# Performance work log

Hardware: AMD Instinct MI355X
Metric: run time of the kernel (lower is better)

## Reference

```python
import jax, jax.numpy as jnp
import numpy as np

N_LAYERS = 8
DILATIONS = [1, 2, 1, 2, 1, 2, 1, 2]
K_HOPS = 3
BN = 13248   # batch(64) * n_nodes(207), merged as in the torch module
L = 13       # 12 history steps + 1; shrinks by sum(dilations)=12 across layers
E = 211968   # BN * avg_degree(16)


def _conv1d(x, w, b, dil):
    # x: (BN, Cin, L), w: (Cout, Cin, 2) kernel-2 dilated conv, VALID (causal shrink)
    y = jax.lax.conv_general_dilated(x, w, (1,), 'VALID', rhs_dilation=(dil,),
                                     dimension_numbers=('NCH', 'OIH', 'NCH'))
    return y + b[None, :, None]


def setup_inputs() -> dict:
    key = jax.random.key(0)
    ks = jax.random.split(key, 20)
    s = 0.1  # keep activations in a sane range
    return {
        'x': jax.random.normal(ks[0], (BN, L, 2), jnp.float32),
        'edge_src': jax.random.randint(ks[1], (E,), 0, BN),
        'edge_dst': jax.random.randint(ks[2], (E,), 0, BN),
        'edge_w': jax.random.uniform(ks[3], (E,), jnp.float32),
        'init_w': s * jax.random.normal(ks[4], (2, 32), jnp.float32),
        'init_b': s * jax.random.normal(ks[5], (32,), jnp.float32),
        'filt_w': s * jax.random.normal(ks[6], (8, 32, 32, 2), jnp.float32),
        'filt_b': s * jax.random.normal(ks[7], (8, 32), jnp.float32),
        'gate_w': s * jax.random.normal(ks[8], (8, 32, 32, 2), jnp.float32),
        'gate_b': s * jax.random.normal(ks[9], (8, 32), jnp.float32),
        'gcn_w': s * jax.random.normal(ks[10], (8, 6, 32, 32), jnp.float32),
        'gcn_b': s * jax.random.normal(ks[11], (8, 32), jnp.float32),
        'skip_w': s * jax.random.normal(ks[12], (8, 256, 32), jnp.float32),
        'skip_b': s * jax.random.normal(ks[13], (8, 256), jnp.float32),
        'out0_w': s * jax.random.normal(ks[14], (256, 512), jnp.float32),
        'out0_b': s * jax.random.normal(ks[15], (512,), jnp.float32),
        'out1_w': s * jax.random.normal(ks[16], (512, 12), jnp.float32),
        'out1_b': s * jax.random.normal(ks[17], (12,), jnp.float32),
    }


def reference(x, edge_src, edge_dst, edge_w, init_w, init_b,
              filt_w, filt_b, gate_w, gate_b, gcn_w, gcn_b,
              skip_w, skip_b, out0_w, out0_b, out1_w, out1_b):
    # init linear: (BN, L, 2) -> (BN, L, 32) -> (BN, 32, L)
    h = (x @ init_w + init_b).transpose(0, 2, 1)
    # per-hop edge weights: elementwise powers of the transition weights
    # (faithful to repo's dense_to_sparse(transition ** k)); bck = transposed edges
    adjs = [(edge_src, edge_dst, edge_w ** k) for k in range(1, K_HOPS + 1)] + \
           [(edge_dst, edge_src, edge_w ** k) for k in range(1, K_HOPS + 1)]
    skip = None
    for l in range(N_LAYERS):
        d = DILATIONS[l]
        res = h
        # Gated TCN: tanh(filter) * sigmoid(gate), seq shrinks by d
        t = jnp.tanh(_conv1d(h, filt_w[l], filt_b[l], d)) * \
            jax.nn.sigmoid(_conv1d(h, gate_w[l], gate_b[l], d))
        # Diffusion conv: sum over 6 adjacency types of A_w (x W_a)
        xt = t.transpose(0, 2, 1)  # (BN, L', 32)
        g = jnp.zeros_like(xt)
        for a, (src, dst, w) in enumerate(adjs):
            msg = (xt @ gcn_w[l, a])[src] * w[:, None, None]  # (E, L', 32)
            g = g + jax.ops.segment_sum(msg, dst, num_segments=BN)
        h = g.transpose(0, 2, 1) + gcn_b[l][None, :, None]  # (BN, 32, L')
        # residual connection (align shrunk sequence)
        h = h + res[:, :, -h.shape[-1]:]
        # skip conv (1x1) on last timestep, accumulated
        sc = h[:, :, -1] @ skip_w[l].T + skip_b[l]  # (BN, 256)
        skip = sc if skip is None else skip + sc
    out = jax.nn.relu(skip)
    out = jax.nn.relu(out @ out0_w + out0_b)
    return out @ out1_w + out1_b  # (BN, 12)
```

## Files before the change

kernel.cpp:

```cpp
#include <hip/hip_runtime.h>
#include <hip/hip_fp16.h>

#define BN 13248
#define NE 211968
#define ZSTRIDE 200
#define HSTRIDE 40
#define HNODE 480

typedef __attribute__((ext_vector_type(8))) short bf16x8;
typedef __attribute__((ext_vector_type(8))) _Float16 f16x8;
typedef __attribute__((ext_vector_type(4))) float f32x4;

__device__ __forceinline__ f32x4 mfma16b(bf16x8 a, bf16x8 b, f32x4 c) {
  return __builtin_amdgcn_mfma_f32_16x16x32_bf16(a, b, c, 0, 0, 0);
}
__device__ __forceinline__ f32x4 mfma16h(f16x8 a, f16x8 b, f32x4 c) {
  return __builtin_amdgcn_mfma_f32_16x16x32_f16(a, b, c, 0, 0, 0);
}

__device__ __forceinline__ unsigned short to_bf16(float v) {
  unsigned bits = __float_as_uint(v);
  return (unsigned short)((bits + 0x7FFFu + ((bits >> 16) & 1u)) >> 16);
}
__device__ __forceinline__ unsigned short to_f16(float v) {
  union { __half h; unsigned short s; } u; u.h = __float2half(v); return u.s;
}
__device__ __forceinline__ unsigned h2u(__half2 h) {
  union { __half2 h; unsigned u; } v; v.h = h; return v.u;
}
__device__ __forceinline__ __half2 u2h(unsigned u) {
  union { unsigned u; __half2 h; } v; v.u = u; return v.h;
}

__device__ __forceinline__ float fast_tanh(float x) {
  float e2 = __expf(2.f * x);
  return 1.f - 2.f / (e2 + 1.f);
}
__device__ __forceinline__ float fast_sig(float x) {
  return 1.f / (1.f + __expf(-x));
}

__global__ void k_count(const int* __restrict__ src, const int* __restrict__ dst,
                        int* __restrict__ cur_f, int* __restrict__ cur_b) {
  int e = blockIdx.x * 256 + threadIdx.x;
  if (e < NE) {
    atomicAdd(&cur_f[dst[e]], 1);
    atomicAdd(&cur_b[src[e]], 1);
  }
}

__global__ void k_scan(int* __restrict__ cur_f, int* __restrict__ row_f,
                       int* __restrict__ cur_b, int* __restrict__ row_b) {
  __shared__ int sdata[1024];
  int tid = threadIdx.x;
  for (int which = 0; which < 2; ++which) {
    int* cnt = which ? cur_b : cur_f;
    int* row = which ? row_b : row_f;
    int base = tid * 13;
    int vals[13];
    int tot = 0;
    for (int k = 0; k < 13; ++k) {
      int idx = base + k;
      int v = (idx < BN) ? cnt[idx] : 0;
      vals[k] = v; tot += v;
    }
    sdata[tid] = tot;
    __syncthreads();
    for (int off = 1; off < 1024; off <<= 1) {
      int add = (tid >= off) ? sdata[tid - off] : 0;
      __syncthreads();
      sdata[tid] += add;
      __syncthreads();
    }
    int running = sdata[tid] - tot;
    for (int k = 0; k < 13; ++k) {
      int idx = base + k;
      if (idx < BN) { row[idx] = running; cnt[idx] = running; running += vals[k]; }
    }
    if (tid == 1023) row[BN] = sdata[1023];
    __syncthreads();
  }
}

__global__ void k_fill(const int* __restrict__ src, const int* __restrict__ dst,
                       const float* __restrict__ w,
                       int* __restrict__ cur_f, int4* __restrict__ ce_f,
                       int* __restrict__ cur_b, int4* __restrict__ ce_b) {
  int e = blockIdx.x * 256 + threadIdx.x;
  if (e < NE) {
    int s = src[e], t = dst[e];
    float wv = w[e];
    float w2 = wv * wv, w3 = w2 * wv;
    int u1 = (int)h2u(__float2half2_rn(wv));
    int u2 = (int)h2u(__float2half2_rn(w2));
    int u3 = (int)h2u(__float2half2_rn(w3));
    int p = atomicAdd(&cur_f[t], 1); ce_f[p] = make_int4(s, u1, u2, u3);
    int q = atomicAdd(&cur_b[s], 1); ce_b[q] = make_int4(t, u1, u2, u3);
  }
}

__global__ void k_init(const float* __restrict__ x, const float* __restrict__ iw,
                       const float* __restrict__ ib, float* __restrict__ h) {
  int idx = blockIdx.x * 256 + threadIdx.x;
  if (idx >= BN * 13 * 32) return;
  int c = idx & 31;
  int r = idx >> 5;
  int n = r % BN;
  int tau = r / BN;
  float x0 = x[(n * 13 + tau) * 2 + 0];
  float x1 = x[(n * 13 + tau) * 2 + 1];
  h[idx] = fmaf(x0, iw[c], fmaf(x1, iw[32 + c], ib[c]));
}

__global__ void k_pack(const float* __restrict__ skip_w, const float* __restrict__ skip_b,
                       const float* __restrict__ w0, const float* __restrict__ w1,
                       const float* __restrict__ gcn_w,
                       const float* __restrict__ filt_w, const float* __restrict__ gate_w,
                       unsigned short* __restrict__ SWb, unsigned short* __restrict__ W0T,
                       unsigned short* __restrict__ W1T, float* __restrict__ bsum,
                       unsigned short* __restrict__ Gg16, unsigned short* __restrict__ WTC) {
  int id = blockIdx.x * 256 + threadIdx.x;
  if (id < 65536) {
    int j = id >> 8, k = id & 255;
    SWb[id] = to_bf16(skip_w[((k >> 5) * 256 + j) * 32 + (k & 31)]);
  }
  if (id < 131072) {
    int jo = id >> 8, k = id & 255;
    W0T[id] = to_bf16(w0[k * 512 + jo]);
  }
  if (id < 8192) {
    int n = id >> 9, k = id & 511;
    W1T[id] = (n < 12) ? to_bf16(w1[k * 12 + n]) : (unsigned short)0;
  }
  if (id < 256) {
    float s = 0.f;
    for (int l = 0; l < 8; ++l) s += skip_b[l * 256 + id];
    bsum[id] = s;
  }
  if (id < 49152) {
    int l = id / 6144, rem = id % 6144;
    int co = rem / 192, k = rem % 192;
    int a = k >> 5, ci = k & 31;
    Gg16[id] = to_f16(gcn_w[((l * 6 + a) * 32 + ci) * 32 + co]);
  }
  if (id < 32768) {
    int l = id >> 12, rem = id & 4095;
    int g = rem >> 11, co = (rem >> 6) & 31, k = rem & 63;
    const float* srcw = (g ? gate_w : filt_w) + l * 2048;
    float v = (k < 32) ? srcw[(co * 32 + k) * 2 + 0] : srcw[(co * 32 + (k - 32)) * 2 + 1];
    WTC[id] = to_f16(v);
  }
}

template<int LIN, int D, int TPAD>
__global__ __launch_bounds__(256) void k_tcn(const float* __restrict__ h_in, unsigned short* __restrict__ t_out,
    const float* __restrict__ fw, const float* __restrict__ fb,
    const float* __restrict__ gw, const float* __restrict__ gb) {
  constexpr int LOUT = LIN - D;
  __shared__ __align__(16) float wq[32 * 32 * 4];
  __shared__ float hl[8][LIN * 32];
  int tid = threadIdx.x;
  for (int f = tid; f < 4096; f += 256) {
    int e = f & 3, co = (f >> 2) & 31, ci = f >> 7;
    const float* srcw = (e < 2) ? fw : gw;
    wq[f] = srcw[(co * 32 + ci) * 2 + (e & 1)];
  }
  int n0 = blockIdx.x * 8;
  for (int i = tid; i < 8 * LIN * 32; i += 256) {
    int c = i & 31, r = i >> 5;
    int nl = r / LIN, tau = r % LIN;
    hl[nl][tau * 32 + c] = h_in[(tau * BN + n0 + nl) * 32 + c];
  }
  __syncthreads();
  int nl = tid >> 5, co = tid & 31;
  int n = n0 + nl;
  float accf[LOUT], accg[LOUT];
  float fbv = fb[co], gbv = gb[co];
#pragma unroll
  for (int j = 0; j < LOUT; ++j) { accf[j] = fbv; accg[j] = gbv; }
#pragma unroll
  for (int ci = 0; ci < 32; ++ci) {
    float4 wv = *(const float4*)&wq[(ci * 32 + co) * 4];
    float xr[LIN];
#pragma unroll
    for (int t = 0; t < LIN; ++t) xr[t] = hl[nl][t * 32 + ci];
#pragma unroll
    for (int j = 0; j < LOUT; ++j) {
      accf[j] = fmaf(xr[j], wv.x, accf[j]);
      accf[j] = fmaf(xr[j + D], wv.y, accf[j]);
      accg[j] = fmaf(xr[j], wv.z, accg[j]);
      accg[j] = fmaf(xr[j + D], wv.w, accg[j]);
    }
  }
#pragma unroll
  for (int j = 0; j < TPAD; ++j) {
    unsigned short v = 0;
    if (j < LOUT) v = to_f16(fast_tanh(accf[j < LOUT ? j : 0]) * fast_sig(accg[j < LOUT ? j : 0]));
    t_out[(n * TPAD + j) * 32 + co] = v;
  }
}

template<int TPAD, int NT>
__device__ __forceinline__ void edge_fma(const int4& c, const uint2 (&u)[NT], __half2* A) {
  __half2 wh0 = u2h((unsigned)c.y), wh1 = u2h((unsigned)c.z), wh2 = u2h((unsigned)c.w);
#pragma unroll
  for (int j = 0; j < NT; ++j) {
    __half2 v0 = u2h(u[j].x), v1 = u2h(u[j].y);
    A[(0 * NT + j) * 2 + 0] = __hfma2(wh0, v0, A[(0 * NT + j) * 2 + 0]);
    A[(0 * NT + j) * 2 + 1] = __hfma2(wh0, v1, A[(0 * NT + j) * 2 + 1]);
    A[(1 * NT + j) * 2 + 0] = __hfma2(wh1, v0, A[(1 * NT + j) * 2 + 0]);
    A[(1 * NT + j) * 2 + 1] = __hfma2(wh1, v1, A[(1 * NT + j) * 2 + 1]);
    A[(2 * NT + j) * 2 + 0] = __hfma2(wh2, v0, A[(2 * NT + j) * 2 + 0]);
    A[(2 * NT + j) * 2 + 1] = __hfma2(wh2, v1, A[(2 * NT + j) * 2 + 1]);
  }
}

template<int TPAD, int NT>
__device__ __forceinline__ void gather_dir(const unsigned short* __restrict__ t_in,
    int e0, int e1, const int4* __restrict__ ce, int rowoff0, __half2* A) {
  constexpr int EB = 4;
  int e = e0;
  for (; e + EB <= e1; e += EB) {
    int4 c[EB];
    uint2 u[EB][NT];
#pragma unroll
    for (int k = 0; k < EB; ++k) c[k] = ce[e + k];
#pragma unroll
    for (int k = 0; k < EB; ++k) {
      const unsigned short* p = t_in + c[k].x * (TPAD * 32) + rowoff0;
#pragma unroll
      for (int j = 0; j < NT; ++j) u[k][j] = *(const uint2*)(p + j * 32);
    }
#pragma unroll
    for (int k = 0; k < EB; ++k) edge_fma<TPAD, NT>(c[k], u[k], A);
  }
  for (; e < e1; ++e) {
    int4 c = ce[e];
    uint2 u[NT];
    const unsigned short* p = t_in + c.x * (TPAD * 32) + rowoff0;
#pragma unroll
    for (int j = 0; j < NT; ++j) u[j] = *(const uint2*)(p + j * 32);
    edge_fma<TPAD, NT>(c, u, A);
  }
}

template<int LOUT, int D, int TPAD, int D2, int TPAD2, bool LAST>
__global__ __launch_bounds__(128, 4) void k_fused(
    const unsigned short* __restrict__ t_in,
    const float* __restrict__ h_in, float* __restrict__ h_out,
    float* __restrict__ lastcol, unsigned short* __restrict__ t_next,
    const int* __restrict__ row_f, const int4* __restrict__ ce_f,
    const int* __restrict__ row_b, const int4* __restrict__ ce_b,
    const unsigned short* __restrict__ Wg,
    const float* __restrict__ bias,
    const unsigned short* __restrict__ Wtc,
    const float* __restrict__ fbn, const float* __restrict__ gbn) {
  constexpr int NT = TPAD / 4;
  constexpr int LOUT2 = LAST ? 1 : (LOUT - D2);
  constexpr int SBYTES = 4 * TPAD * ZSTRIDE * 2;
  __shared__ __align__(16) char smem[SBYTES];
  unsigned short* Zl = (unsigned short*)smem;
  unsigned short* hb16 = (unsigned short*)smem;
  int tid = threadIdx.x;
  int nl = tid >> 5, lane32 = tid & 31;
  int tl = lane32 >> 3;
  int c4 = (lane32 & 7) << 2;
  int n0 = blockIdx.x * 4;
  int n = n0 + nl;
  int rowoff0 = (tl * NT) * 32 + c4;
  int ef0 = row_f[n], ef1 = row_f[n + 1];
  int eb0 = row_b[n], eb1 = row_b[n + 1];
  __half2 acc[6 * NT * 2];
  __half2 zero = __float2half2_rn(0.f);
#pragma unroll
  for (int i = 0; i < 6 * NT * 2; ++i) acc[i] = zero;
  gather_dir<TPAD, NT>(t_in, ef0, ef1, ce_f, rowoff0, acc);
  gather_dir<TPAD, NT>(t_in, eb0, eb1, ce_b, rowoff0, acc + 3 * NT * 2);
#pragma unroll
  for (int j = 0; j < NT; ++j) {
    int m = nl * TPAD + tl * NT + j;
#pragma unroll
    for (int a = 0; a < 6; ++a) {
      uint2 v = make_uint2(h2u(acc[(a * NT + j) * 2 + 0]), h2u(acc[(a * NT + j) * 2 + 1]));
      *(uint2*)(&Zl[m * ZSTRIDE + a * 32 + c4]) = v;
    }
  }
  __syncthreads();
  int wave = tid >> 6, lane = tid & 63;
  int m16 = lane & 15, q = lane >> 4;
  f32x4 dacc[NT];
#pragma unroll
  for (int i = 0; i < NT; ++i) {
    int u = wave * NT + i;
    int mt = u >> 1, nt = u & 1;
    dacc[i] = (f32x4){0.f, 0.f, 0.f, 0.f};
#pragma unroll
    for (int ks = 0; ks < 6; ++ks) {
      f16x8 av = *(const f16x8*)(&Zl[(mt * 16 + m16) * ZSTRIDE + ks * 32 + q * 8]);
      f16x8 bv = *(const f16x8*)((const _Float16*)Wg + (nt * 16 + m16) * 192 + ks * 32 + q * 8);
      dacc[i] = mfma16h(av, bv, dacc[i]);
    }
  }
  __syncthreads();
#pragma unroll
  for (int i = 0; i < NT; ++i) {
    int u = wave * NT + i;
    int mt = u >> 1, nt = u & 1;
    int co = nt * 16 + m16;
    float bco = bias[co];
#pragma unroll
    for (int r = 0; r < 4; ++r) {
      int mm = mt * 16 + q * 4 + r;
      int node = mm / TPAD;
      int tau = mm % TPAD;
      if (tau < LOUT) {
        float rres = h_in[((tau + D) * BN + n0 + node) * 32 + co];
        float o = dacc[i][r] + bco + rres;
        h_out[(tau * BN + n0 + node) * 32 + co] = o;
        if (!LAST) hb16[node * HNODE + tau * HSTRIDE + co] = to_f16(o);
        if (tau == LOUT - 1) lastcol[(n0 + node) * 32 + co] = o;
      }
    }
  }
  if (!LAST) {
    __syncthreads();
#pragma unroll
    for (int i = 0; i < 4; ++i) {
      int u = wave * 4 + i;
      int node = u >> 1, ntc = u & 1;
      int co = ntc * 16 + m16;
      f32x4 df = (f32x4){0.f, 0.f, 0.f, 0.f};
      f32x4 dg = (f32x4){0.f, 0.f, 0.f, 0.f};
#pragma unroll
      for (int s = 0; s < 2; ++s) {
        f16x8 av = *(const f16x8*)(&hb16[node * HNODE + (m16 + s * D2) * HSTRIDE + q * 8]);
        f16x8 bvf = *(const f16x8*)((const _Float16*)Wtc + (0 * 32 + co) * 64 + s * 32 + q * 8);
        f16x8 bvg = *(const f16x8*)((const _Float16*)Wtc + (1 * 32 + co) * 64 + s * 32 + q * 8);
        df = mfma16h(av, bvf, df);
        dg = mfma16h(av, bvg, dg);
      }
      float fbv = fbn[co], gbv = gbn[co];
#pragma unroll
      for (int r = 0; r < 4; ++r) {
        int j = q * 4 + r;
        if (j < TPAD2) {
          unsigned short v = 0;
          if (j < LOUT2)
            v = to_f16(fast_tanh(df[r] + fbv) * fast_sig(dg[r] + gbv));
          t_next[((n0 + node) * TPAD2 + j) * 32 + co] = v;
        }
      }
    }
  }
}

__device__ __forceinline__ bf16x8 ldsA(const unsigned short* buf, int stride, int row, int ks, int q) {
  int unit = ks * 4 + q;
  int addr = row * stride + ((unit ^ (row & 7)) << 3);
  return *(const bf16x8*)(buf + addr);
}

__global__ __launch_bounds__(256) void k_final(const float* __restrict__ lastcol,
    const unsigned short* __restrict__ SWb, const unsigned short* __restrict__ W0T,
    const unsigned short* __restrict__ W1T, const float* __restrict__ bsum,
    const float* __restrict__ b0, const float* __restrict__ b1,
    float* __restrict__ out) {
  __shared__ __align__(16) unsigned short Z[32 * 256];
  __shared__ __align__(16) unsigned short H[32 * 512];
  int tid = threadIdx.x;
  int wave = tid >> 6, lane = tid & 63;
  int m16 = lane & 15, q = lane >> 4;
  int n0 = blockIdx.x * 32;
#pragma unroll
  for (int it = 0; it < 32; ++it) {
    int id = it * 256 + tid;
    int m = id >> 8, k = id & 255;
    float v = lastcol[((k >> 5) * BN + n0 + m) * 32 + (k & 31)];
    Z[m * 256 + (((k >> 3) ^ (m & 7)) << 3) + (k & 7)] = to_bf16(v);
  }
  __syncthreads();
  f32x4 acc1[2][4];
#pragma unroll
  for (int mt = 0; mt < 2; ++mt)
#pragma unroll
    for (int i = 0; i < 4; ++i) acc1[mt][i] = (f32x4){0.f, 0.f, 0.f, 0.f};
#pragma unroll
  for (int ks = 0; ks < 8; ++ks) {
    bf16x8 a0 = ldsA(Z, 256, m16, ks, q);
    bf16x8 a1 = ldsA(Z, 256, 16 + m16, ks, q);
#pragma unroll
    for (int i = 0; i < 4; ++i) {
      int j = (wave * 4 + i) * 16 + m16;
      bf16x8 b = *(const bf16x8*)(SWb + j * 256 + ks * 32 + q * 8);
      acc1[0][i] = mfma16b(a0, b, acc1[0][i]);
      acc1[1][i] = mfma16b(a1, b, acc1[1][i]);
    }
  }
  __syncthreads();
#pragma unroll
  for (int i = 0; i < 4; ++i) {
    int j = (wave * 4 + i) * 16 + m16;
    float bs = bsum[j];
#pragma unroll
    for (int mt = 0; mt < 2; ++mt)
#pragma unroll
      for (int r = 0; r < 4; ++r) {
        int row = mt * 16 + q * 4 + r;
        float v = fmaxf(acc1[mt][i][r] + bs, 0.f);
        Z[row * 256 + (((j >> 3) ^ (row & 7)) << 3) + (j & 7)] = to_bf16(v);
      }
  }
  __syncthreads();
  f32x4 acc2[2][8];
#pragma unroll
  for (int mt = 0; mt < 2; ++mt)
#pragma unroll
    for (int i = 0; i < 8; ++i) acc2[mt][i] = (f32x4){0.f, 0.f, 0.f, 0.f};
#pragma unroll
  for (int ks = 0; ks < 8; ++ks) {
    bf16x8 a0 = ldsA(Z, 256, m16, ks, q);
    bf16x8 a1 = ldsA(Z, 256, 16 + m16, ks, q);
#pragma unroll
    for (int i = 0; i < 8; ++i) {
      int jo = (wave * 8 + i) * 16 + m16;
      bf16x8 b = *(const bf16x8*)(W0T + jo * 256 + ks * 32 + q * 8);
      acc2[0][i] = mfma16b(a0, b, acc2[0][i]);
      acc2[1][i] = mfma16b(a1, b, acc2[1][i]);
    }
  }
#pragma unroll
  for (int i = 0; i < 8; ++i) {
    int jo = (wave * 8 + i) * 16 + m16;
    float b0v = b0[jo];
#pragma unroll
    for (int mt = 0; mt < 2; ++mt)
#pragma unroll
      for (int r = 0; r < 4; ++r) {
        int row = mt * 16 + q * 4 + r;
        float v = fmaxf(acc2[mt][i][r] + b0v, 0.f);
        H[row * 512 + (((jo >> 3) ^ (row & 7)) << 3) + (jo & 7)] = to_bf16(v);
      }
  }
  __syncthreads();
  if (wave < 2) {
    f32x4 acc3 = (f32x4){0.f, 0.f, 0.f, 0.f};
#pragma unroll
    for (int ks = 0; ks < 16; ++ks) {
      bf16x8 a = ldsA(H, 512, wave * 16 + m16, ks, q);
      bf16x8 b = *(const bf16x8*)(W1T + m16 * 512 + ks * 32 + q * 8);
      acc3 = mfma16b(a, b, acc3);
    }
    if (m16 < 12) {
      float bv = b1[m16];
#pragma unroll
      for (int r = 0; r < 4; ++r)
        out[(n0 + wave * 16 + q * 4 + r) * 12 + m16] = acc3[r] + bv;
    }
  }
}

extern "C" void kernel_launch(void* const* d_in, const int* in_sizes, int n_in,
                              void* d_out, int out_size, void* d_ws, size_t ws_size,
                              hipStream_t stream) {
  const float* x      = (const float*)d_in[0];
  const int*   esrc   = (const int*)d_in[1];
  const int*   edst   = (const int*)d_in[2];
  const float* ew     = (const float*)d_in[3];
  const float* init_w = (const float*)d_in[4];
  const float* init_b = (const float*)d_in[5];
  const float* filt_w = (const float*)d_in[6];
  const float* filt_b = (const float*)d_in[7];
  const float* gate_w = (const float*)d_in[8];
  const float* gate_b = (const float*)d_in[9];
  const float* gcn_w  = (const float*)d_in[10];
  const float* gcn_b  = (const float*)d_in[11];
  const float* skip_w = (const float*)d_in[12];
  const float* skip_b = (const float*)d_in[13];
  const float* w0     = (const float*)d_in[14];
  const float* b0     = (const float*)d_in[15];
  const float* w1     = (const float*)d_in[16];
  const float* b1     = (const float*)d_in[17];
  float* out = (float*)d_out;

  float* base = (float*)d_ws;
  float* hA      = base;
  float* hB      = hA + 13 * BN * 32;
  unsigned short* tA = (unsigned short*)(hB + 13 * BN * 32);
  unsigned short* tB = tA + 12 * BN * 32;
  float* lastcol = (float*)(tB + 12 * BN * 32);
  int* row_f = (int*)(lastcol + 8 * BN * 32);
  int* row_b = row_f + (BN + 2);
  int* cur_f = row_b + (BN + 2);
  int* cur_b = cur_f + BN;
  int4* ce_f = (int4*)(cur_b + BN + 2);
  int4* ce_b = ce_f + NE;
  unsigned short* SWb  = (unsigned short*)(ce_b + NE);
  unsigned short* W0T  = SWb + 65536;
  unsigned short* W1T  = W0T + 131072;
  unsigned short* Gg16 = W1T + 8192;
  unsigned short* WTC  = Gg16 + 49152;
  float* bsumv = (float*)(WTC + 32768);

  hipMemsetAsync(cur_f, 0, 2 * BN * sizeof(int), stream);
  const int egrid = (NE + 255) / 256;
  k_count<<<egrid, 256, 0, stream>>>(esrc, edst, cur_f, cur_b);
  k_scan<<<1, 1024, 0, stream>>>(cur_f, row_f, cur_b, row_b);
  k_fill<<<egrid, 256, 0, stream>>>(esrc, edst, ew, cur_f, ce_f, cur_b, ce_b);
  k_init<<<(BN * 13 * 32 + 255) / 256, 256, 0, stream>>>(x, init_w, init_b, hA);
  k_pack<<<512, 256, 0, stream>>>(skip_w, skip_b, w0, w1, gcn_w, filt_w, gate_w,
                                  SWb, W0T, W1T, bsumv, Gg16, WTC);

  k_tcn<13, 1, 12><<<BN / 8, 256, 0, stream>>>(hA, tA, filt_w, filt_b, gate_w, gate_b);

#define FUSED(l, LOUTv, Dv, TPv, D2v, TP2v, LASTv, tin, tout, hin, hout) \
  k_fused<LOUTv, Dv, TPv, D2v, TP2v, LASTv><<<BN / 4, 128, 0, stream>>>( \
      tin, hin, hout, lastcol + l * BN * 32, tout, row_f, ce_f, row_b, ce_b, \
      Gg16 + l * 6144, gcn_b + l * 32, WTC + (l + 1) * 4096, \
      filt_b + (l + 1) * 32, gate_b + (l + 1) * 32);

  FUSED(0, 12, 1, 12, 2, 12, false, tA, tB, hA, hB)
  FUSED(1, 10, 2, 12, 1, 12, false, tB, tA, hB, hA)
  FUSED(2,  9, 1, 12, 2,  8, false, tA, tB, hA, hB)
  FUSED(3,  7, 2,  8, 1,  8, false, tB, tA, hB, hA)
  FUSED(4,  6, 1,  8, 2,  4, false, tA, tB, hA, hB)
  FUSED(5,  4, 2,  4, 1,  4, false, tB, tA, hB, hA)
  FUSED(6,  3, 1,  4, 2,  4, false, tA, tB, hA, hB)
#undef FUSED
  k_fused<1, 2, 4, 2, 4, true><<<BN / 4, 128, 0, stream>>>(
      tB, hB, hA, lastcol + 7 * BN * 32, tA, row_f, ce_f, row_b, ce_b,
      Gg16 + 7 * 6144, gcn_b + 7 * 32, WTC, filt_b, gate_b);

  k_final<<<BN / 32, 256, 0, stream>>>(lastcol, SWb, W0T, W1T, bsumv, b0, b1, out);
}
```

Baseline: 684.3 us.

## Bucket CSR edges by neighbor index range and skip padded row loads

Edge counting, scan and fill now use 8 sub-buckets per node keyed by the high bits of the neighbor index, so each node's edge list is roughly sorted by source node. This should make the gathers in the fused layer kernels touch memory with better locality and L2 reuse. The gather also skips loading padded time rows beyond the valid output length when the padded size exceeds it. In exchange the scan runs over 8x more counters in a single block, and the count and fill atomics are spread over a larger array.

```diff
diff --git a/kernel.cpp b/kernel.cpp
--- a/kernel.cpp
+++ b/kernel.cpp
@@ -3,6 +3,7 @@
 
 #define BN 13248
 #define NE 211968
+#define NBKT 8
 #define ZSTRIDE 200
 #define HSTRIDE 40
 #define HNODE 480
@@ -44,25 +45,26 @@
                         int* __restrict__ cur_f, int* __restrict__ cur_b) {
   int e = blockIdx.x * 256 + threadIdx.x;
   if (e < NE) {
-    atomicAdd(&cur_f[dst[e]], 1);
-    atomicAdd(&cur_b[src[e]], 1);
-  }
-}
-
-__global__ void k_scan(int* __restrict__ cur_f, int* __restrict__ row_f,
-                       int* __restrict__ cur_b, int* __restrict__ row_b) {
+    int s = src[e], t = dst[e];
+    atomicAdd(&cur_f[t * NBKT + (s >> 11)], 1);
+    atomicAdd(&cur_b[s * NBKT + (t >> 11)], 1);
+  }
+}
+
+__global__ void k_scan(int* __restrict__ cnt_f, int* __restrict__ row_f,
+                       int* __restrict__ cnt_b, int* __restrict__ row_b) {
   __shared__ int sdata[1024];
+  const int TOT = BN * NBKT;
+  const int PER = (TOT + 1023) / 1024;
   int tid = threadIdx.x;
   for (int which = 0; which < 2; ++which) {
-    int* cnt = which ? cur_b : cur_f;
+    int* cnt = which ? cnt_b : cnt_f;
     int* row = which ? row_b : row_f;
-    int base = tid * 13;
-    int vals[13];
+    int base = tid * PER;
     int tot = 0;
-    for (int k = 0; k < 13; ++k) {
+    for (int k = 0; k < PER; ++k) {
       int idx = base + k;
-      int v = (idx < BN) ? cnt[idx] : 0;
-      vals[k] = v; tot += v;
+      if (idx < TOT) tot += cnt[idx];
     }
     sdata[tid] = tot;
     __syncthreads();
@@ -73,11 +75,16 @@
       __syncthreads();
     }
     int running = sdata[tid] - tot;
-    for (int k = 0; k < 13; ++k) {
+    for (int k = 0; k < PER; ++k) {
       int idx = base + k;
-      if (idx < BN) { row[idx] = running; cnt[idx] = running; running += vals[k]; }
-    }
-    if (tid == 1023) row[BN] = sdata[1023];
+      if (idx < TOT) {
+        int v = cnt[idx];
+        if ((idx & (NBKT - 1)) == 0) row[idx / NBKT] = running;
+        cnt[idx] = running;
+        running += v;
+      }
+    }
+    if (tid == 1023) row[BN] = NE;
     __syncthreads();
   }
 }
@@ -94,8 +101,8 @@
     int u1 = (int)h2u(__float2half2_rn(wv));
     int u2 = (int)h2u(__float2half2_rn(w2));
     int u3 = (int)h2u(__float2half2_rn(w3));
-    int p = atomicAdd(&cur_f[t], 1); ce_f[p] = make_int4(s, u1, u2, u3);
-    int q = atomicAdd(&cur_b[s], 1); ce_b[q] = make_int4(t, u1, u2, u3);
+    int p = atomicAdd(&cur_f[t * NBKT + (s >> 11)], 1); ce_f[p] = make_int4(s, u1, u2, u3);
+    int q = atomicAdd(&cur_b[s * NBKT + (t >> 11)], 1); ce_b[q] = make_int4(t, u1, u2, u3);
   }
 }
 
@@ -215,9 +222,10 @@
   }
 }
 
-template<int TPAD, int NT>
+template<int TPAD, int NT, int LOUTT>
 __device__ __forceinline__ void gather_dir(const unsigned short* __restrict__ t_in,
-    int e0, int e1, const int4* __restrict__ ce, int rowoff0, __half2* A) {
+    int e0, int e1, const int4* __restrict__ ce, int rowoff0, int rowbase, __half2* A) {
+  constexpr bool FULL = (LOUTT >= TPAD);
   constexpr int EB = 4;
   int e = e0;
   for (; e + EB <= e1; e += EB) {
@@ -229,7 +237,10 @@
     for (int k = 0; k < EB; ++k) {
       const unsigned short* p = t_in + c[k].x * (TPAD * 32) + rowoff0;
 #pragma unroll
-      for (int j = 0; j < NT; ++j) u[k][j] = *(const uint2*)(p + j * 32);
+      for (int j = 0; j < NT; ++j) {
+        if (FULL || rowbase + j < LOUTT) u[k][j] = *(const uint2*)(p + j * 32);
+        else u[k][j] = make_uint2(0u, 0u);
+      }
     }
 #pragma unroll
     for (int k = 0; k < EB; ++k) edge_fma<TPAD, NT>(c[k], u[k], A);
@@ -239,7 +250,10 @@
     uint2 u[NT];
     const unsigned short* p = t_in + c.x * (TPAD * 32) + rowoff0;
 #pragma unroll
-    for (int j = 0; j < NT; ++j) u[j] = *(const uint2*)(p + j * 32);
+    for (int j = 0; j < NT; ++j) {
+      if (FULL || rowbase + j < LOUTT) u[j] = *(const uint2*)(p + j * 32);
+      else u[j] = make_uint2(0u, 0u);
+    }
     edge_fma<TPAD, NT>(c, u, A);
   }
 }
@@ -267,18 +281,19 @@
   int c4 = (lane32 & 7) << 2;
   int n0 = blockIdx.x * 4;
   int n = n0 + nl;
-  int rowoff0 = (tl * NT) * 32 + c4;
+  int rowbase = tl * NT;
+  int rowoff0 = rowbase * 32 + c4;
   int ef0 = row_f[n], ef1 = row_f[n + 1];
   int eb0 = row_b[n], eb1 = row_b[n + 1];
   __half2 acc[6 * NT * 2];
   __half2 zero = __float2half2_rn(0.f);
 #pragma unroll
   for (int i = 0; i < 6 * NT * 2; ++i) acc[i] = zero;
-  gather_dir<TPAD, NT>(t_in, ef0, ef1, ce_f, rowoff0, acc);
-  gather_dir<TPAD, NT>(t_in, eb0, eb1, ce_b, rowoff0, acc + 3 * NT * 2);
+  gather_dir<TPAD, NT, LOUT>(t_in, ef0, ef1, ce_f, rowoff0, rowbase, acc);
+  gather_dir<TPAD, NT, LOUT>(t_in, eb0, eb1, ce_b, rowoff0, rowbase, acc + 3 * NT * 2);
 #pragma unroll
   for (int j = 0; j < NT; ++j) {
-    int m = nl * TPAD + tl * NT + j;
+    int m = nl * TPAD + rowbase + j;
 #pragma unroll
     for (int a = 0; a < 6; ++a) {
       uint2 v = make_uint2(h2u(acc[(a * NT + j) * 2 + 0]), h2u(acc[(a * NT + j) * 2 + 1]));
@@ -491,8 +506,8 @@
   int* row_f = (int*)(lastcol + 8 * BN * 32);
   int* row_b = row_f + (BN + 2);
   int* cur_f = row_b + (BN + 2);
-  int* cur_b = cur_f + BN;
-  int4* ce_f = (int4*)(cur_b + BN + 2);
+  int* cur_b = cur_f + BN * NBKT;
+  int4* ce_f = (int4*)(cur_b + BN * NBKT);
   int4* ce_b = ce_f + NE;
   unsigned short* SWb  = (unsigned short*)(ce_b + NE);
   unsigned short* W0T  = SWb + 65536;
@@ -501,7 +516,7 @@
   unsigned short* WTC  = Gg16 + 49152;
   float* bsumv = (float*)(WTC + 32768);
 
-  hipMemsetAsync(cur_f, 0, 2 * BN * sizeof(int), stream);
+  hipMemsetAsync(cur_f, 0, 2 * BN * NBKT * sizeof(int), stream);
   const int egrid = (NE + 255) / 256;
   k_count<<<egrid, 256, 0, stream>>>(esrc, edst, cur_f, cur_b);
   k_scan<<<1, 1024, 0, stream>>>(cur_f, row_f, cur_b, row_b);
```

New measurement: 1.002 ms. 46.4% more time.
